# Kernel tuning notes

Measured on AMD Instinct MI355X. Metric: run time of the kernel, lower is better.

## Reference

```python
import jax, jax.numpy as jnp
from jax import lax
import numpy as np

C = 12        # input channels
H = 233       # lstm hidden
L = 6         # lstm layers
P = 96        # sliding window length
F = 96        # forecast steps
B = 16        # batch (treated as SEQ axis by the LSTM, matching the torch code)


def setup_inputs() -> dict:
    key = jax.random.key(0)
    ks = jax.random.split(key, 9)
    s = 1.0 / np.sqrt(H)  # pytorch default uniform init scale
    u = lambda k, shape: jax.random.uniform(k, shape, jnp.float32, -s, s)
    return {
        "X": jax.random.normal(ks[0], (B, P, C), jnp.float32),
        "Wih0": u(ks[1], (4 * H, C)),        # layer 0 input weights
        "Wih": u(ks[2], (L - 1, 4 * H, H)),  # layers 1..5 input weights
        "Whh": u(ks[3], (L, 4 * H, H)),
        "bih": u(ks[4], (L, 4 * H)),
        "bhh": u(ks[5], (L, 4 * H)),
        "Wl": u(ks[6], (C, H)),
        "bl": u(ks[7], (C,)),
    }


def _lstm_layer(x, wih, whh, b):
    # x: (S, N, in) -> (S, N, H); scan over seq axis 0, gate order i,f,g,o (pytorch)
    N = x.shape[1]
    h0 = jnp.zeros((N, H), x.dtype)

    def cell(carry, xt):
        h, c = carry
        gates = xt @ wih.T + h @ whh.T + b          # (N, 4H)
        i, f, g, o = jnp.split(gates, 4, axis=-1)
        c = jax.nn.sigmoid(f) * c + jax.nn.sigmoid(i) * jnp.tanh(g)
        h = jax.nn.sigmoid(o) * jnp.tanh(c)
        return (h, c), h

    _, ys = lax.scan(cell, (h0, h0), x)
    return ys


def reference(X, Wih0, Wih, Whh, bih, bhh, Wl, bl):
    # Faithful to torch: nn.LSTM without batch_first treats axis0=B as seq,
    # axis1=P as batch; output[0][:, -1, :] picks the last window position.
    def step(window, _):
        x = _lstm_layer(window, Wih0, Whh[0], bih[0] + bhh[0])
        for l in range(1, L):
            x = _lstm_layer(x, Wih[l - 1], Whh[l], bih[l] + bhh[l])
        h_last = x[:, -1, :]              # (B, H)
        new = h_last @ Wl.T + bl          # (B, C)
        window = jnp.concatenate([window[:, 1:, :], new[:, None, :]], axis=1)
        return window, new

    _, toks = lax.scan(step, X, None, length=F)   # (F, B, C)
    return jnp.transpose(toks, (1, 0, 2))          # (B, F, C)
```

## Files before the change

kernel.cpp:

```cpp
#include <hip/hip_runtime.h>

#define HND    233
#define NL     6
#define GPL    15
#define UPW    16
#define ROWS   64
#define TSTEPS 16
#define FSTEPS 96
#define NSLOT  (TSTEPS*FSTEPS)
#define CDIM   12
#define G4H    (4*HND)
#define HP     240
#define VINW   496
#define NTICK  (6*95+15+1)
#define NHEAD  3
#define BLOCK  256
#define NWORD  234
#define AG     __HIP_MEMORY_SCOPE_AGENT
#define SENT   0x7FBADBADu

typedef unsigned long long u64;

__device__ __forceinline__ float sigf(float x) { return 1.f / (1.f + expf(-x)); }
__device__ __forceinline__ bool rdy(u64 v) {
  return ((unsigned)v != SENT) && ((unsigned)(v >> 32) != SENT);
}

__global__ void init_kernel(unsigned* __restrict__ hout, int hp) {
  size_t i = (size_t)blockIdx.x * blockDim.x + threadIdx.x;
  size_t stride = (size_t)gridDim.x * blockDim.x;
  const size_t nh = (size_t)NL * NSLOT * hp;
  for (size_t k = i; k < nh; k += stride) hout[k] = ((int)(k % hp) < HND) ? SENT : 0u;
}

__global__ void __launch_bounds__(BLOCK, 1) lstm_pipe(
    const float* __restrict__ X,
    const float* __restrict__ Wih0, const float* __restrict__ Wih,
    const float* __restrict__ Whh,  const float* __restrict__ bih,
    const float* __restrict__ bhh,  const float* __restrict__ Wl,
    const float* __restrict__ bl,   float* __restrict__ out,
    float* __restrict__ hout, int hps ) {
  __shared__ float vin[3][VINW];
  __shared__ float part[3][BLOCK];
  __shared__ float bias[ROWS];
  __shared__ float cst[3][UPW];
  __shared__ float wih0s[ROWS][CDIM];
  __shared__ float xs[TSTEPS][CDIM];
  __shared__ float wlh[CDIM][HP];

  const int tid = threadIdx.x;
  const int bid = blockIdx.x;
  u64* hu = (u64*)hout;

  if (bid >= NL * GPL) {
    const int hid = bid - NL * GPL;
    for (int i = tid; i < CDIM * HP; i += BLOCK) {
      int rr = i / HP, k = i % HP;
      ((float*)wlh)[i] = (k < HND) ? Wl[rr * HND + k] : 0.f;
    }
    for (int i = tid; i < VINW; i += BLOCK) vin[0][i] = 0.f;
    __syncthreads();
    for (int f = hid; f < FSTEPS; f += NHEAD) {
      for (int t = 0; t < TSTEPS; ++t) {
        const u64* src = hu + ((size_t)5 * NSLOT + 16 * f + t) * hps;
        if (tid < 117) {
          u64 v; long gd = 0;
          for (;;) {
            v = __hip_atomic_load(src + tid, __ATOMIC_RELAXED, AG);
            if (rdy(v)) break;
            if (++gd > (1L << 20)) break;
            if (gd > 4) __builtin_amdgcn_s_sleep(1);
          }
          *(u64*)&vin[0][2 * tid] = v;
        }
        __syncthreads();
        if (tid < 48) {
          int rr = tid >> 2, q = tid & 3;
          const float4* wr = (const float4*)&wlh[rr][0];
          const float4* hv = (const float4*)&vin[0][0];
          float a = 0.f;
          #pragma unroll
          for (int c = 0; c < 15; ++c) {
            float4 x0 = wr[q * 15 + c], y0 = hv[q * 15 + c];
            a = fmaf(x0.w, y0.w, fmaf(x0.z, y0.z, fmaf(x0.y, y0.y, fmaf(x0.x, y0.x, a))));
          }
          a += __shfl_xor(a, 1);
          a += __shfl_xor(a, 2);
          if (q == 0) out[((size_t)t * FSTEPS + f) * CDIM + rr] = a + bl[rr];
        }
        __syncthreads();
      }
    }
    return;
  }

  const int l = bid / GPL, g = bid % GPL;
  const int j0 = g * UPW;
  const int U = min(UPW, HND - j0);
  const int r = tid & 63, q = tid >> 6;
  const int u = r >> 2, gt = r & 3;
  const int grow = gt * HND + j0 + u;
  const bool rowok = (u < U);

  if (l == 0) {
    for (int i = tid; i < CDIM * HP; i += BLOCK) {
      int rr = i / HP, k = i % HP;
      ((float*)wlh)[i] = (k < HND) ? Wl[rr * HND + k] : 0.f;
    }
    for (int i = tid; i < ROWS * CDIM; i += BLOCK) {
      int rr = i / CDIM, c = i % CDIM;
      int uu = rr >> 2, g2 = rr & 3;
      wih0s[rr][c] = (uu < U) ? Wih0[(g2 * HND + j0 + uu) * CDIM + c] : 0.f;
    }
    for (int i = tid; i < TSTEPS * CDIM; i += BLOCK)
      xs[i / CDIM][i % CDIM] = X[((size_t)(i / CDIM) * 96 + 95) * CDIM + (i % CDIM)];
  }
  for (int i = tid; i < 3 * VINW; i += BLOCK) ((float*)vin)[i] = 0.f;
  __syncthreads();

  float4 w4[31];
  const float* wihl = Wih + (size_t)(l - 1) * G4H * HND;
  const float* whhl = Whh + (size_t)l * G4H * HND;
  #pragma unroll
  for (int j = 0; j < 31; ++j) {
    float e[4];
    #pragma unroll
    for (int ee = 0; ee < 4; ++ee) {
      const int idx = (q * 31 + j) * 4 + ee;
      float v = 0.f;
      if (rowok) {
        if (idx < HND) {
          if (l == 0) {
            float acc = 0.f;
            #pragma unroll
            for (int c = 0; c < CDIM; ++c) acc = fmaf(wih0s[r][c], wlh[c][idx], acc);
            v = acc;
          } else {
            v = wihl[(size_t)grow * HND + idx];
          }
        } else if (idx >= HP && idx < HP + HND) {
          v = whhl[(size_t)grow * HND + (idx - HP)];
        }
      }
      e[ee] = v;
    }
    w4[j] = make_float4(e[0], e[1], e[2], e[3]);
  }
  if (tid < ROWS) {
    float b = 0.f;
    if (rowok) {
      b = bih[l * G4H + grow] + bhh[l * G4H + grow];
      if (l == 0) {
        #pragma unroll
        for (int c = 0; c < CDIM; ++c) b = fmaf(wih0s[tid][c], bl[c], b);
      }
    }
    bias[tid] = b;
  }
  __syncthreads();

  long glimit = 1L << 20;
  for (int m = 0; m < NTICK; ++m) {
    const int fh0 = m / 6;
    const int f_hi = (fh0 > 95) ? 95 : fh0;
    const int f_lo = (m < 10) ? 0 : (m - 10) / 6;

    const u64 *s0 = nullptr, *s1 = nullptr, *s2 = nullptr;
    u64 *d0 = nullptr, *d1 = nullptr, *d2 = nullptr;

    auto setup = [&](int w, const u64*& sp, u64*& dp) {
      const int k = w / NWORD;
      const int f = f_lo + k;
      if (f > f_hi) return;
      const int t = m - 6 * f;
      const int o = w - k * NWORD;
      if (o < 117) {
        if (l == 0 && f == 0) {
          vin[k][2 * o]     = (2 * o     < CDIM) ? xs[t][2 * o]     : 0.f;
          vin[k][2 * o + 1] = (2 * o + 1 < CDIM) ? xs[t][2 * o + 1] : 0.f;
          return;
        }
        sp = (l == 0)
           ? hu + ((size_t)5 * NSLOT + 16 * (f - 1) + t) * hps + o
           : hu + ((size_t)(l - 1) * NSLOT + 16 * f + t) * hps + o;
        dp = (u64*)&vin[k][2 * o];
      } else {
        const int jj = o - 117;
        if (t == 0) {
          vin[k][HP + 2 * jj] = 0.f; vin[k][HP + 2 * jj + 1] = 0.f;
          return;
        }
        sp = hu + ((size_t)l * NSLOT + 16 * f + t - 1) * hps + jj;
        dp = (u64*)&vin[k][HP + 2 * jj];
      }
    };
    setup(tid, s0, d0);
    setup(tid + 256, s1, d1);
    if (tid + 512 < 3 * NWORD) setup(tid + 512, s2, d2);

    long gd = 0;
    while (s0 || s1 || s2) {
      if (s0) { u64 v = __hip_atomic_load(s0, __ATOMIC_RELAXED, AG); if (rdy(v)) { *d0 = v; s0 = nullptr; } }
      if (s1) { u64 v = __hip_atomic_load(s1, __ATOMIC_RELAXED, AG); if (rdy(v)) { *d1 = v; s1 = nullptr; } }
      if (s2) { u64 v = __hip_atomic_load(s2, __ATOMIC_RELAXED, AG); if (rdy(v)) { *d2 = v; s2 = nullptr; } }
      if (++gd > glimit) { glimit = 64; break; }
      if (gd > 8) __builtin_amdgcn_s_sleep(1);
    }
    __syncthreads();

    const float4* va = (const float4*)&vin[0][0];
    const float4* vb = (const float4*)&vin[1][0];
    const float4* vc = (const float4*)&vin[2][0];
    float a0 = 0.f, a1 = 0.f, a2 = 0.f;
    #pragma unroll
    for (int j = 0; j < 31; ++j) {
      const int c = q * 31 + j;
      const float4 wv = w4[j];
      const float4 y0 = va[c];
      a0 = fmaf(wv.x, y0.x, fmaf(wv.y, y0.y, fmaf(wv.z, y0.z, fmaf(wv.w, y0.w, a0))));
      const float4 y1 = vb[c];
      a1 = fmaf(wv.x, y1.x, fmaf(wv.y, y1.y, fmaf(wv.z, y1.z, fmaf(wv.w, y1.w, a1))));
      const float4 y2 = vc[c];
      a2 = fmaf(wv.x, y2.x, fmaf(wv.y, y2.y, fmaf(wv.z, y2.z, fmaf(wv.w, y2.w, a2))));
    }
    part[0][tid] = a0; part[1][tid] = a1; part[2][tid] = a2;
    __syncthreads();

    if (tid < 48) {
      const int k = tid >> 4, uu = tid & 15;
      const int f = f_lo + k;
      const bool act = (f <= f_hi);
      float hn = 0.f;
      int t = 0;
      if (act) {
        t = m - 6 * f;
        const int b3 = f % 3;
        float gg[4];
        #pragma unroll
        for (int g2 = 0; g2 < 4; ++g2) {
          const int rr = 4 * uu + g2;
          float s = part[k][rr] + part[k][rr + 64] + part[k][rr + 128] +
                    part[k][rr + 192] + bias[rr];
          if (l == 0 && f == 0) {
            #pragma unroll
            for (int c = 0; c < CDIM; ++c) s = fmaf(wih0s[rr][c], xs[t][c], s);
          }
          gg[g2] = s;
        }
        if (uu < U) {
          const float cp = (t == 0) ? 0.f : cst[b3][uu];
          const float cn = sigf(gg[1]) * cp + sigf(gg[0]) * tanhf(gg[2]);
          hn = sigf(gg[3]) * tanhf(cn);
          cst[b3][uu] = cn;
        }
      }
      const float hi = __shfl(hn, tid | 1);
      if (act && (uu & 1) == 0 && uu < U) {
        const u64 pv = ((u64)__float_as_uint(hi) << 32) | (u64)__float_as_uint(hn);
        __hip_atomic_store(hu + ((size_t)l * NSLOT + 16 * f + t) * hps + (j0 >> 1) + (uu >> 1),
                           pv, __ATOMIC_RELAXED, AG);
      }
    }
  }
}

extern "C" void kernel_launch(void* const* d_in, const int* in_sizes, int n_in,
                              void* d_out, int out_size, void* d_ws, size_t ws_size,
                              hipStream_t stream) {
  const float* X    = (const float*)d_in[0];
  const float* Wih0 = (const float*)d_in[1];
  const float* Wih  = (const float*)d_in[2];
  const float* Whh  = (const float*)d_in[3];
  const float* bih  = (const float*)d_in[4];
  const float* bhh  = (const float*)d_in[5];
  const float* Wl   = (const float*)d_in[6];
  const float* bl   = (const float*)d_in[7];

  size_t need240 = (size_t)NL * NSLOT * 240 * 4;
  const int hp = (ws_size >= need240) ? 240 : 234;
  float* hout = (float*)d_ws;

  init_kernel<<<2048, 256, 0, stream>>>((unsigned*)hout, hp);
  lstm_pipe<<<NL * GPL + NHEAD, BLOCK, 0, stream>>>(
      X, Wih0, Wih, Whh, bih, bhh, Wl, bl, (float*)d_out, hout, hp / 2);
}
```

Measured before the change: 2.236 ms.

## Add per-slot completion counters for LSTM pipeline sync and skip idle slot dot products

Adds an integer counter per (layer, slot) that each producer block increments after storing its hidden-state chunk. Consumers poll up to six counters until all 15 producer groups have reported, instead of relying only on per-word sentinel spinning. The per-word sentinel check is kept, so correctness does not depend on store ordering across threads. Matvec passes for the second and third in-flight slots are skipped when fewer slots are active. This adds an extra atomic round trip and a vmcnt wait every tick, and it enlarges the workspace requirement.

```diff
diff --git a/kernel.cpp b/kernel.cpp
--- a/kernel.cpp
+++ b/kernel.cpp
@@ -26,11 +26,12 @@
   return ((unsigned)v != SENT) && ((unsigned)(v >> 32) != SENT);
 }
 
-__global__ void init_kernel(unsigned* __restrict__ hout, int hp) {
+__global__ void init_kernel(unsigned* __restrict__ hout, int* __restrict__ cnt, int hp) {
   size_t i = (size_t)blockIdx.x * blockDim.x + threadIdx.x;
   size_t stride = (size_t)gridDim.x * blockDim.x;
   const size_t nh = (size_t)NL * NSLOT * hp;
   for (size_t k = i; k < nh; k += stride) hout[k] = ((int)(k % hp) < HND) ? SENT : 0u;
+  for (size_t k = i; k < (size_t)NL * NSLOT; k += stride) cnt[k] = 0;
 }
 
 __global__ void __launch_bounds__(BLOCK, 1) lstm_pipe(
@@ -39,7 +40,7 @@
     const float* __restrict__ Whh,  const float* __restrict__ bih,
     const float* __restrict__ bhh,  const float* __restrict__ Wl,
     const float* __restrict__ bl,   float* __restrict__ out,
-    float* __restrict__ hout, int hps ) {
+    float* __restrict__ hout, int* __restrict__ cnt, int hps) {
   __shared__ float vin[3][VINW];
   __shared__ float part[3][BLOCK];
   __shared__ float bias[ROWS];
@@ -62,14 +63,23 @@
     __syncthreads();
     for (int f = hid; f < FSTEPS; f += NHEAD) {
       for (int t = 0; t < TSTEPS; ++t) {
-        const u64* src = hu + ((size_t)5 * NSLOT + 16 * f + t) * hps;
+        const int slot = 16 * f + t;
+        {
+          const int* cp = cnt + 5 * NSLOT + slot;
+          long gd = 0;
+          while (__hip_atomic_load(cp, __ATOMIC_RELAXED, AG) < GPL) {
+            if (++gd > (1L << 20)) break;
+            if (gd > 2) __builtin_amdgcn_s_sleep(1);
+          }
+        }
         if (tid < 117) {
+          const u64* src = hu + ((size_t)5 * NSLOT + slot) * hps + tid;
           u64 v; long gd = 0;
           for (;;) {
-            v = __hip_atomic_load(src + tid, __ATOMIC_RELAXED, AG);
+            v = __hip_atomic_load(src, __ATOMIC_RELAXED, AG);
             if (rdy(v)) break;
             if (++gd > (1L << 20)) break;
-            if (gd > 4) __builtin_amdgcn_s_sleep(1);
+            if (gd > 2) __builtin_amdgcn_s_sleep(1);
           }
           *(u64*)&vin[0][2 * tid] = v;
         }
@@ -159,11 +169,42 @@
   }
   __syncthreads();
 
-  long glimit = 1L << 20;
   for (int m = 0; m < NTICK; ++m) {
     const int fh0 = m / 6;
     const int f_hi = (fh0 > 95) ? 95 : fh0;
     const int f_lo = (m < 10) ? 0 : (m - 10) / 6;
+    const int nk = f_hi - f_lo + 1;
+
+    {
+      const int* cw[6] = {nullptr, nullptr, nullptr, nullptr, nullptr, nullptr};
+      #pragma unroll
+      for (int k = 0; k < 3; ++k) {
+        const int f = f_lo + k;
+        if (f <= f_hi) {
+          const int t = m - 6 * f;
+          if (l == 0) {
+            if (f > 0) cw[2 * k] = cnt + 5 * NSLOT + 16 * (f - 1) + t;
+          } else {
+            cw[2 * k] = cnt + (l - 1) * NSLOT + 16 * f + t;
+          }
+          if (t > 0) cw[2 * k + 1] = cnt + l * NSLOT + 16 * f + (t - 1);
+        }
+      }
+      long gd = 0;
+      for (;;) {
+        bool miss = false;
+        #pragma unroll
+        for (int i = 0; i < 6; ++i) {
+          if (cw[i]) {
+            if (__hip_atomic_load(cw[i], __ATOMIC_RELAXED, AG) >= GPL) cw[i] = nullptr;
+            else miss = true;
+          }
+        }
+        if (!miss) break;
+        if (++gd > (1L << 20)) break;
+        if (gd > 2) __builtin_amdgcn_s_sleep(1);
+      }
+    }
 
     const u64 *s0 = nullptr, *s1 = nullptr, *s2 = nullptr;
     u64 *d0 = nullptr, *d1 = nullptr, *d2 = nullptr;
@@ -203,8 +244,8 @@
       if (s0) { u64 v = __hip_atomic_load(s0, __ATOMIC_RELAXED, AG); if (rdy(v)) { *d0 = v; s0 = nullptr; } }
       if (s1) { u64 v = __hip_atomic_load(s1, __ATOMIC_RELAXED, AG); if (rdy(v)) { *d1 = v; s1 = nullptr; } }
       if (s2) { u64 v = __hip_atomic_load(s2, __ATOMIC_RELAXED, AG); if (rdy(v)) { *d2 = v; s2 = nullptr; } }
-      if (++gd > glimit) { glimit = 64; break; }
-      if (gd > 8) __builtin_amdgcn_s_sleep(1);
+      if (++gd > (1L << 20)) break;
+      if (gd > 4) __builtin_amdgcn_s_sleep(1);
     }
     __syncthreads();
 
@@ -218,10 +259,24 @@
       const float4 wv = w4[j];
       const float4 y0 = va[c];
       a0 = fmaf(wv.x, y0.x, fmaf(wv.y, y0.y, fmaf(wv.z, y0.z, fmaf(wv.w, y0.w, a0))));
-      const float4 y1 = vb[c];
-      a1 = fmaf(wv.x, y1.x, fmaf(wv.y, y1.y, fmaf(wv.z, y1.z, fmaf(wv.w, y1.w, a1))));
-      const float4 y2 = vc[c];
-      a2 = fmaf(wv.x, y2.x, fmaf(wv.y, y2.y, fmaf(wv.z, y2.z, fmaf(wv.w, y2.w, a2))));
+    }
+    if (nk > 1) {
+      #pragma unroll
+      for (int j = 0; j < 31; ++j) {
+        const int c = q * 31 + j;
+        const float4 wv = w4[j];
+        const float4 y1 = vb[c];
+        a1 = fmaf(wv.x, y1.x, fmaf(wv.y, y1.y, fmaf(wv.z, y1.z, fmaf(wv.w, y1.w, a1))));
+      }
+    }
+    if (nk > 2) {
+      #pragma unroll
+      for (int j = 0; j < 31; ++j) {
+        const int c = q * 31 + j;
+        const float4 wv = w4[j];
+        const float4 y2 = vc[c];
+        a2 = fmaf(wv.x, y2.x, fmaf(wv.y, y2.y, fmaf(wv.z, y2.z, fmaf(wv.w, y2.w, a2))));
+      }
     }
     part[0][tid] = a0; part[1][tid] = a1; part[2][tid] = a2;
     __syncthreads();
@@ -261,6 +316,12 @@
                            pv, __ATOMIC_RELAXED, AG);
       }
     }
+    asm volatile("s_waitcnt vmcnt(0)" ::: "memory");
+    if (tid < 48 && (tid & 15) == 0) {
+      const int k = tid >> 4, f = f_lo + k;
+      if (f <= f_hi)
+        __hip_atomic_fetch_add(cnt + l * NSLOT + 10 * f + m, 1, __ATOMIC_RELAXED, AG);
+    }
   }
 }
 
@@ -276,11 +337,12 @@
   const float* Wl   = (const float*)d_in[6];
   const float* bl   = (const float*)d_in[7];
 
-  size_t need240 = (size_t)NL * NSLOT * 240 * 4;
+  size_t need240 = (size_t)NL * NSLOT * 240 * 4 + (size_t)NL * NSLOT * 4;
   const int hp = (ws_size >= need240) ? 240 : 234;
   float* hout = (float*)d_ws;
-
-  init_kernel<<<2048, 256, 0, stream>>>((unsigned*)hout, hp);
+  int* cnt = (int*)(hout + (size_t)NL * NSLOT * hp);
+
+  init_kernel<<<2048, 256, 0, stream>>>((unsigned*)hout, cnt, hp);
   lstm_pipe<<<NL * GPL + NHEAD, BLOCK, 0, stream>>>(
-      X, Wih0, Wih, Whh, bih, bhh, Wl, bl, (float*)d_out, hout, hp / 2);
+      X, Wih0, Wih, Whh, bih, bhh, Wl, bl, (float*)d_out, hout, cnt, hp / 2);
 }
```

Measured after the change: 4.205 ms. +88.0%, slower.

## Widen LSTM blocks to 32 units, add per-group ready flags, skip idle dot products

Applied to the files above, without the earlier changes.

Each layer is now split into 8 groups of 32 hidden units, run by 512-thread blocks instead of 15 groups of 16 units with 256 threads. This halves the number of producer blocks each consumer has to wait on. A per-slot, per-group ready counter array is added in workspace. Consumers first spin on at most 8 flags, then read the h vectors, so most of the polling no longer hammers the sentinel-tagged data. The three pipeline dot products now only run for active forecast slots, which trims idle FMAs during ramp-up and ramp-down. The trade-off is fewer blocks doing twice the work each, one extra flag store per step, and more workspace use.

```diff
diff --git a/kernel.cpp b/kernel.cpp
--- a/kernel.cpp
+++ b/kernel.cpp
@@ -2,9 +2,9 @@
 
 #define HND    233
 #define NL     6
-#define GPL    15
-#define UPW    16
-#define ROWS   64
+#define GPL    8
+#define UPW    32
+#define ROWS   128
 #define TSTEPS 16
 #define FSTEPS 96
 #define NSLOT  (TSTEPS*FSTEPS)
@@ -14,7 +14,7 @@
 #define VINW   496
 #define NTICK  (6*95+15+1)
 #define NHEAD  3
-#define BLOCK  256
+#define BLOCK  512
 #define NWORD  234
 #define AG     __HIP_MEMORY_SCOPE_AGENT
 #define SENT   0x7FBADBADu
@@ -26,11 +26,12 @@
   return ((unsigned)v != SENT) && ((unsigned)(v >> 32) != SENT);
 }
 
-__global__ void init_kernel(unsigned* __restrict__ hout, int hp) {
+__global__ void init_kernel(unsigned* __restrict__ hout, int* __restrict__ cny, int hp) {
   size_t i = (size_t)blockIdx.x * blockDim.x + threadIdx.x;
   size_t stride = (size_t)gridDim.x * blockDim.x;
   const size_t nh = (size_t)NL * NSLOT * hp;
   for (size_t k = i; k < nh; k += stride) hout[k] = ((int)(k % hp) < HND) ? SENT : 0u;
+  for (size_t k = i; k < (size_t)NL * NSLOT * GPL; k += stride) cny[k] = 0;
 }
 
 __global__ void __launch_bounds__(BLOCK, 1) lstm_pipe(
@@ -39,7 +40,7 @@
     const float* __restrict__ Whh,  const float* __restrict__ bih,
     const float* __restrict__ bhh,  const float* __restrict__ Wl,
     const float* __restrict__ bl,   float* __restrict__ out,
-    float* __restrict__ hout, int hps ) {
+    float* __restrict__ hout, int* __restrict__ cny, int hps) {
   __shared__ float vin[3][VINW];
   __shared__ float part[3][BLOCK];
   __shared__ float bias[ROWS];
@@ -62,14 +63,15 @@
     __syncthreads();
     for (int f = hid; f < FSTEPS; f += NHEAD) {
       for (int t = 0; t < TSTEPS; ++t) {
-        const u64* src = hu + ((size_t)5 * NSLOT + 16 * f + t) * hps;
+        const int slot = 16 * f + t;
         if (tid < 117) {
+          const u64* src = hu + ((size_t)5 * NSLOT + slot) * hps + tid;
           u64 v; long gd = 0;
           for (;;) {
-            v = __hip_atomic_load(src + tid, __ATOMIC_RELAXED, AG);
+            v = __hip_atomic_load(src, __ATOMIC_RELAXED, AG);
             if (rdy(v)) break;
             if (++gd > (1L << 20)) break;
-            if (gd > 4) __builtin_amdgcn_s_sleep(1);
+            if (gd > 2) __builtin_amdgcn_s_sleep(1);
           }
           *(u64*)&vin[0][2 * tid] = v;
         }
@@ -97,7 +99,7 @@
   const int l = bid / GPL, g = bid % GPL;
   const int j0 = g * UPW;
   const int U = min(UPW, HND - j0);
-  const int r = tid & 63, q = tid >> 6;
+  const int r = tid & 127, q = tid >> 7;
   const int u = r >> 2, gt = r & 3;
   const int grow = gt * HND + j0 + u;
   const bool rowok = (u < U);
@@ -118,15 +120,15 @@
   for (int i = tid; i < 3 * VINW; i += BLOCK) ((float*)vin)[i] = 0.f;
   __syncthreads();
 
-  float4 w4[31];
+  float4 w4[30];
   const float* wihl = Wih + (size_t)(l - 1) * G4H * HND;
   const float* whhl = Whh + (size_t)l * G4H * HND;
   #pragma unroll
-  for (int j = 0; j < 31; ++j) {
+  for (int j = 0; j < 30; ++j) {
     float e[4];
     #pragma unroll
     for (int ee = 0; ee < 4; ++ee) {
-      const int idx = (q * 31 + j) * 4 + ee;
+      const int idx = (q * 30 + j) * 4 + ee;
       float v = 0.f;
       if (rowok) {
         if (idx < HND) {
@@ -159,14 +161,44 @@
   }
   __syncthreads();
 
-  long glimit = 1L << 20;
   for (int m = 0; m < NTICK; ++m) {
     const int fh0 = m / 6;
     const int f_hi = (fh0 > 95) ? 95 : fh0;
     const int f_lo = (m < 10) ? 0 : (m - 10) / 6;
-
-    const u64 *s0 = nullptr, *s1 = nullptr, *s2 = nullptr;
-    u64 *d0 = nullptr, *d1 = nullptr, *d2 = nullptr;
+    const int nk = f_hi - f_lo + 1;
+
+    {
+      const int* cp = nullptr;
+      if (tid < 48) {
+        const int gi = tid >> 3, g2 = tid & 7;
+        const int k = gi >> 1;
+        const bool isx = (gi & 1) == 0;
+        const int f = f_lo + k;
+        if (f <= f_hi) {
+          const int t = m - 6 * f;
+          if (isx) {
+            if (l == 0) {
+              if (f > 0) cp = cny + ((size_t)5 * NSLOT + 16 * (f - 1) + t) * GPL + g2;
+            } else {
+              cp = cny + ((size_t)(l - 1) * NSLOT + 16 * f + t) * GPL + g2;
+            }
+          } else if (t > 0) {
+            cp = cny + ((size_t)l * NSLOT + 16 * f + t - 1) * GPL + g2;
+          }
+        }
+      }
+      if (cp) {
+        long gd = 0;
+        while (__hip_atomic_load(cp, __ATOMIC_RELAXED, AG) == 0) {
+          if (++gd > (1L << 20)) break;
+          if (gd > 8) __builtin_amdgcn_s_sleep(1);
+        }
+      }
+      __syncthreads();
+    }
+
+    const u64 *s0 = nullptr, *s1 = nullptr;
+    u64 *d0 = nullptr, *d1 = nullptr;
 
     auto setup = [&](int w, const u64*& sp, u64*& dp) {
       const int k = w / NWORD;
@@ -195,16 +227,14 @@
       }
     };
     setup(tid, s0, d0);
-    setup(tid + 256, s1, d1);
-    if (tid + 512 < 3 * NWORD) setup(tid + 512, s2, d2);
+    if (tid + BLOCK < 3 * NWORD) setup(tid + BLOCK, s1, d1);
 
     long gd = 0;
-    while (s0 || s1 || s2) {
+    while (s0 || s1) {
       if (s0) { u64 v = __hip_atomic_load(s0, __ATOMIC_RELAXED, AG); if (rdy(v)) { *d0 = v; s0 = nullptr; } }
       if (s1) { u64 v = __hip_atomic_load(s1, __ATOMIC_RELAXED, AG); if (rdy(v)) { *d1 = v; s1 = nullptr; } }
-      if (s2) { u64 v = __hip_atomic_load(s2, __ATOMIC_RELAXED, AG); if (rdy(v)) { *d2 = v; s2 = nullptr; } }
-      if (++gd > glimit) { glimit = 64; break; }
-      if (gd > 8) __builtin_amdgcn_s_sleep(1);
+      if (++gd > (1L << 20)) break;
+      if (gd > 4) __builtin_amdgcn_s_sleep(1);
     }
     __syncthreads();
 
@@ -213,21 +243,35 @@
     const float4* vc = (const float4*)&vin[2][0];
     float a0 = 0.f, a1 = 0.f, a2 = 0.f;
     #pragma unroll
-    for (int j = 0; j < 31; ++j) {
-      const int c = q * 31 + j;
+    for (int j = 0; j < 30; ++j) {
+      const int c = q * 30 + j;
       const float4 wv = w4[j];
       const float4 y0 = va[c];
       a0 = fmaf(wv.x, y0.x, fmaf(wv.y, y0.y, fmaf(wv.z, y0.z, fmaf(wv.w, y0.w, a0))));
-      const float4 y1 = vb[c];
-      a1 = fmaf(wv.x, y1.x, fmaf(wv.y, y1.y, fmaf(wv.z, y1.z, fmaf(wv.w, y1.w, a1))));
-      const float4 y2 = vc[c];
-      a2 = fmaf(wv.x, y2.x, fmaf(wv.y, y2.y, fmaf(wv.z, y2.z, fmaf(wv.w, y2.w, a2))));
+    }
+    if (nk > 1) {
+      #pragma unroll
+      for (int j = 0; j < 30; ++j) {
+        const int c = q * 30 + j;
+        const float4 wv = w4[j];
+        const float4 y1 = vb[c];
+        a1 = fmaf(wv.x, y1.x, fmaf(wv.y, y1.y, fmaf(wv.z, y1.z, fmaf(wv.w, y1.w, a1))));
+      }
+    }
+    if (nk > 2) {
+      #pragma unroll
+      for (int j = 0; j < 30; ++j) {
+        const int c = q * 30 + j;
+        const float4 wv = w4[j];
+        const float4 y2 = vc[c];
+        a2 = fmaf(wv.x, y2.x, fmaf(wv.y, y2.y, fmaf(wv.z, y2.z, fmaf(wv.w, y2.w, a2))));
+      }
     }
     part[0][tid] = a0; part[1][tid] = a1; part[2][tid] = a2;
     __syncthreads();
 
-    if (tid < 48) {
-      const int k = tid >> 4, uu = tid & 15;
+    if (tid < 96) {
+      const int k = tid >> 5, uu = tid & 31;
       const int f = f_lo + k;
       const bool act = (f <= f_hi);
       float hn = 0.f;
@@ -239,8 +283,8 @@
         #pragma unroll
         for (int g2 = 0; g2 < 4; ++g2) {
           const int rr = 4 * uu + g2;
-          float s = part[k][rr] + part[k][rr + 64] + part[k][rr + 128] +
-                    part[k][rr + 192] + bias[rr];
+          float s = part[k][rr] + part[k][rr + 128] + part[k][rr + 256] +
+                    part[k][rr + 384] + bias[rr];
           if (l == 0 && f == 0) {
             #pragma unroll
             for (int c = 0; c < CDIM; ++c) s = fmaf(wih0s[rr][c], xs[t][c], s);
@@ -248,18 +292,21 @@
           gg[g2] = s;
         }
         if (uu < U) {
-          const float cp = (t == 0) ? 0.f : cst[b3][uu];
-          const float cn = sigf(gg[1]) * cp + sigf(gg[0]) * tanhf(gg[2]);
+          const float cp2 = (t == 0) ? 0.f : cst[b3][uu];
+          const float cn = sigf(gg[1]) * cp2 + sigf(gg[0]) * tanhf(gg[2]);
           hn = sigf(gg[3]) * tanhf(cn);
           cst[b3][uu] = cn;
         }
       }
-      const float hi = __shfl(hn, tid | 1);
+      const float hi = __shfl(hn, (tid & 63) | 1);
       if (act && (uu & 1) == 0 && uu < U) {
         const u64 pv = ((u64)__float_as_uint(hi) << 32) | (u64)__float_as_uint(hn);
         __hip_atomic_store(hu + ((size_t)l * NSLOT + 16 * f + t) * hps + (j0 >> 1) + (uu >> 1),
                            pv, __ATOMIC_RELAXED, AG);
       }
+      if (act && uu == 0)
+        __hip_atomic_store(cny + ((size_t)l * NSLOT + 10 * f + m) * GPL + g, 1,
+                           __ATOMIC_RELAXED, AG);
     }
   }
 }
@@ -276,11 +323,13 @@
   const float* Wl   = (const float*)d_in[6];
   const float* bl   = (const float*)d_in[7];
 
-  size_t need240 = (size_t)NL * NSLOT * 240 * 4;
+  const size_t cnyN = (size_t)NL * NSLOT * GPL;
+  size_t need240 = (size_t)NL * NSLOT * 240 * 4 + cnyN * 4;
   const int hp = (ws_size >= need240) ? 240 : 234;
   float* hout = (float*)d_ws;
-
-  init_kernel<<<2048, 256, 0, stream>>>((unsigned*)hout, hp);
+  int* cny = (int*)(hout + (size_t)NL * NSLOT * hp);
+
+  init_kernel<<<2048, 256, 0, stream>>>((unsigned*)hout, cny, hp);
   lstm_pipe<<<NL * GPL + NHEAD, BLOCK, 0, stream>>>(
-      X, Wih0, Wih, Whh, bih, bhh, Wl, bl, (float*)d_out, hout, hp / 2);
+      X, Wih0, Wih, Whh, bih, bhh, Wl, bl, (float*)d_out, hout, cny, hp / 2);
 }
```

Result: slower. 4.799 ms (+114.6%).
